# Performance work log

Hardware: AMD Instinct MI355X
Metric: run time of the kernel (lower is better)

## Reference

```python
import jax, jax.numpy as jnp
import numpy as np

B, N_IN, N_MFS, N_RULES = 8192, 8, 4, 2048


def setup_inputs() -> dict:
    key = jax.random.key(0)
    k1, k2 = jax.random.split(key)
    # fuzzified membership values in [0, 1): (n_cases, n_in, n_mfs)
    x = jax.random.uniform(k1, (B, N_IN, N_MFS), dtype=jnp.float32)
    # rule MF-index table: values in [-1, n_mfs-1]; -1 means 'variable unused in rule'
    mf_indices = jax.random.randint(k2, (N_RULES, N_IN), 0, N_MFS + 1, dtype=jnp.int32) - 1
    return {"x": x, "mf_indices": mf_indices}


def reference(x, mf_indices):
    """AntecedentLayer.forward, rules path with AND_p (product t-norm).
    x:          (B, n_in, n_mfs)
    mf_indices: (n_rules, n_in), -1 = masked
    returns fire strengths: (B, n_rules)
    """
    cond = mf_indices == -1                      # (R, n_in)
    safe_idx = jnp.where(cond, 0, mf_indices)    # clamp sentinel for gather
    n_in = x.shape[1]
    # ants[b, r, i] = x[b, i, safe_idx[r, i]]  -> (B, R, n_in)
    ants = x[:, jnp.arange(n_in)[None, :], safe_idx]
    # masked variables contribute identity (1.0) to the product t-norm
    ants = jnp.where(cond[None, :, :], jnp.float32(1.0), ants)
    return jnp.prod(ants, axis=2)                # (B, R)
```

## Files before the change

kernel.cpp:

```cpp
#include <hip/hip_runtime.h>

#define B        8192
#define N_IN     8
#define N_MFS    4
#define N_RULES  2048

#define THREADS  256
#define NB       16
#define LUT_W    101

typedef float vfloat4 __attribute__((ext_vector_type(4)));

__global__ __launch_bounds__(THREADS) void fire_kernel(
        const float* __restrict__ x,
        const int*   __restrict__ mf,
        float* __restrict__ out)
{
    __shared__ float slut[NB * LUT_W];

    const int tid = threadIdx.x;
    const int b0  = blockIdx.x * NB;

    int woff[2][4][4];
#pragma unroll
    for (int pass = 0; pass < 2; ++pass) {
#pragma unroll
        for (int j = 0; j < 4; ++j) {
            const int r = pass * (THREADS * 4) + tid * 4 + j;
            const int4* mr = (const int4*)(mf + r * N_IN);
            const int4 lo = mr[0];
            const int4 hi = mr[1];
            const int idx[8] = {lo.x, lo.y, lo.z, lo.w, hi.x, hi.y, hi.z, hi.w};
#pragma unroll
            for (int p = 0; p < 4; ++p) {
                const int a = idx[2*p]   < 0 ? 4 : idx[2*p];
                const int b = idx[2*p+1] < 0 ? 4 : idx[2*p+1];
                woff[pass][j][p] = p * 25 + a * 5 + b;
            }
        }
    }

    for (int e = tid; e < NB * 100; e += THREADS) {
        const int bl   = e / 100;
        const int rest = e - bl * 100;
        const int p    = rest / 25;
        const int c    = rest - p * 25;
        const int a    = c / 5;
        const int bb   = c - a * 5;
        const float* xb = x + (size_t)(b0 + bl) * (N_IN * N_MFS);
        const float va = (a  < 4) ? xb[(2*p)   * N_MFS + a ] : 1.0f;
        const float vb = (bb < 4) ? xb[(2*p+1) * N_MFS + bb] : 1.0f;
        slut[bl * LUT_W + rest] = va * vb;
    }
    __syncthreads();

#pragma unroll
    for (int bl = 0; bl < NB; ++bl) {
#pragma unroll
        for (int pass = 0; pass < 2; ++pass) {
            vfloat4 res;
            float* o = out + (size_t)(b0 + bl) * N_RULES + pass * (THREADS * 4) + tid * 4;
#pragma unroll
            for (int j = 0; j < 4; ++j) {
                const float v0 = slut[bl * LUT_W + woff[pass][j][0]];
                const float v1 = slut[bl * LUT_W + woff[pass][j][1]];
                const float v2 = slut[bl * LUT_W + woff[pass][j][2]];
                const float v3 = slut[bl * LUT_W + woff[pass][j][3]];
                res[j] = (v0 * v1) * (v2 * v3);
            }
            __builtin_nontemporal_store(res, (vfloat4*)o);
        }
    }
}

extern "C" void kernel_launch(void* const* d_in, const int* in_sizes, int n_in,
                              void* d_out, int out_size, void* d_ws, size_t ws_size,
                              hipStream_t stream) {
    const float* x  = (const float*)d_in[0];
    const int*   mf = (const int*)d_in[1];
    float* out = (float*)d_out;
    (void)d_ws; (void)ws_size;

    fire_kernel<<<B / NB, THREADS, 0, stream>>>(x, mf, out);
}
```

Before: 84.33 us.

## Split rules across a 2D grid with one rule per thread and stage x in LDS

New measurement: 80.88 us. -4.1%, faster.

```diff
diff --git a/kernel.cpp b/kernel.cpp
--- a/kernel.cpp
+++ b/kernel.cpp
@@ -6,39 +6,45 @@
 #define N_RULES  2048
 
 #define THREADS  256
-#define NB       16
+#define NB       32
+#define RSPLIT   8
+#define RPB      (N_RULES / RSPLIT)
 #define LUT_W    101
-
-typedef float vfloat4 __attribute__((ext_vector_type(4)));
+#define XS_W     (N_IN * N_MFS)
 
 __global__ __launch_bounds__(THREADS) void fire_kernel(
         const float* __restrict__ x,
         const int*   __restrict__ mf,
         float* __restrict__ out)
 {
+    __shared__ float xs[NB * XS_W];
     __shared__ float slut[NB * LUT_W];
 
     const int tid = threadIdx.x;
-    const int b0  = blockIdx.x * NB;
+    const int rg  = blockIdx.x;
+    const int bg  = blockIdx.y;
+    const int b0  = bg * NB;
+    const int r   = rg * RPB + tid;
 
-    int woff[2][4][4];
+    {
+        const float4* xg = (const float4*)(x + (size_t)b0 * XS_W);
+        ((float4*)xs)[tid] = xg[tid];
+    }
+
+    int woff[4];
+    {
+        const int4* mr = (const int4*)(mf + (size_t)r * N_IN);
+        const int4 lo = mr[0];
+        const int4 hi = mr[1];
+        const int idx[8] = {lo.x, lo.y, lo.z, lo.w, hi.x, hi.y, hi.z, hi.w};
 #pragma unroll
-    for (int pass = 0; pass < 2; ++pass) {
-#pragma unroll
-        for (int j = 0; j < 4; ++j) {
-            const int r = pass * (THREADS * 4) + tid * 4 + j;
-            const int4* mr = (const int4*)(mf + r * N_IN);
-            const int4 lo = mr[0];
-            const int4 hi = mr[1];
-            const int idx[8] = {lo.x, lo.y, lo.z, lo.w, hi.x, hi.y, hi.z, hi.w};
-#pragma unroll
-            for (int p = 0; p < 4; ++p) {
-                const int a = idx[2*p]   < 0 ? 4 : idx[2*p];
-                const int b = idx[2*p+1] < 0 ? 4 : idx[2*p+1];
-                woff[pass][j][p] = p * 25 + a * 5 + b;
-            }
+        for (int p = 0; p < 4; ++p) {
+            const int a = idx[2*p]   < 0 ? 4 : idx[2*p];
+            const int b = idx[2*p+1] < 0 ? 4 : idx[2*p+1];
+            woff[p] = p * 25 + a * 5 + b;
         }
     }
+    __syncthreads();
 
     for (int e = tid; e < NB * 100; e += THREADS) {
         const int bl   = e / 100;
@@ -47,29 +53,23 @@
         const int c    = rest - p * 25;
         const int a    = c / 5;
         const int bb   = c - a * 5;
-        const float* xb = x + (size_t)(b0 + bl) * (N_IN * N_MFS);
+        const float* xb = xs + bl * XS_W;
         const float va = (a  < 4) ? xb[(2*p)   * N_MFS + a ] : 1.0f;
         const float vb = (bb < 4) ? xb[(2*p+1) * N_MFS + bb] : 1.0f;
         slut[bl * LUT_W + rest] = va * vb;
     }
     __syncthreads();
 
-#pragma unroll
+    float* o = out + (size_t)b0 * N_RULES + r;
+#pragma unroll 8
     for (int bl = 0; bl < NB; ++bl) {
-#pragma unroll
-        for (int pass = 0; pass < 2; ++pass) {
-            vfloat4 res;
-            float* o = out + (size_t)(b0 + bl) * N_RULES + pass * (THREADS * 4) + tid * 4;
-#pragma unroll
-            for (int j = 0; j < 4; ++j) {
-                const float v0 = slut[bl * LUT_W + woff[pass][j][0]];
-                const float v1 = slut[bl * LUT_W + woff[pass][j][1]];
-                const float v2 = slut[bl * LUT_W + woff[pass][j][2]];
-                const float v3 = slut[bl * LUT_W + woff[pass][j][3]];
-                res[j] = (v0 * v1) * (v2 * v3);
-            }
-            __builtin_nontemporal_store(res, (vfloat4*)o);
-        }
+        const float* lb = slut + bl * LUT_W;
+        const float v0 = lb[woff[0]];
+        const float v1 = lb[woff[1]];
+        const float v2 = lb[woff[2]];
+        const float v3 = lb[woff[3]];
+        const float res = (v0 * v1) * (v2 * v3);
+        __builtin_nontemporal_store(res, o + (size_t)bl * N_RULES);
     }
 }
 
@@ -81,5 +81,6 @@
     float* out = (float*)d_out;
     (void)d_ws; (void)ws_size;
 
-    fire_kernel<<<B / NB, THREADS, 0, stream>>>(x, mf, out);
+    dim3 grid(RSPLIT, B / NB);
+    fire_kernel<<<grid, THREADS, 0, stream>>>(x, mf, out);
 }
```
